# Kernel tuning notes

Measured on AMD Instinct MI355X. Metric: run time of the kernel, lower is better.

Reference implementation:

```python
import jax, jax.numpy as jnp
import numpy as np

SIZE = 128
BATCH = 64
STEEPNESS = 10.0


def _odd_even_indices(n):
    """Odd-even transposition sorting network: n layers of disjoint adjacent pairs.
    All layers are padded to k = n//2 pairs with self-pairs (i,i)=(0,0), which are
    exact no-ops under the soft compare-exchange (matches pass-through wires of the
    original network)."""
    k = n // 2
    ia, ib = [], []
    for layer in range(n):
        start = layer % 2
        pa = list(range(start, n - 1, 2))
        pb = [i + 1 for i in pa]
        while len(pa) < k:  # pad with no-op self-pairs
            pa.append(0)
            pb.append(0)
        ia.append(pa)
        ib.append(pb)
    return jnp.asarray(np.array(ia, np.int32)), jnp.asarray(np.array(ib, np.int32))


def setup_inputs() -> dict:
    key = jax.random.key(0)
    return {"vectors": jax.random.normal(key, (BATCH, SIZE), dtype=jnp.float32)}


def _soft_sort(vectors):
    Bsz, n = vectors.shape
    ia, ib = _odd_even_indices(n)  # [n_layers, k] each
    x0 = vectors
    # X[b, i, j] = soft probability mass of input element i at output slot j,
    # i.e. the invariant  x[b] == vectors[b] @ X[b]  holds after every layer.
    X0 = jnp.tile(jnp.eye(n, dtype=vectors.dtype)[None], (Bsz, 1, 1))
    inv_pi = jnp.float32(1.0 / np.pi)

    def step(carry, idx):
        x, X = carry
        a_idx, b_idx = idx
        a = x[:, a_idx]  # [B, k]
        b = x[:, b_idx]  # [B, k]
        # Cauchy CDF relaxation of the comparison (module default distribution)
        alpha = jnp.arctan(STEEPNESS * (b - a)) * inv_pi + 0.5
        x = x.at[:, a_idx].set(alpha * a + (1.0 - alpha) * b)        # soft min
        x = x.at[:, b_idx].set((1.0 - alpha) * a + alpha * b)        # soft max
        A = X[:, :, a_idx]   # [B, n, k] columns feeding the 'a' wires
        Bc = X[:, :, b_idx]  # [B, n, k] columns feeding the 'b' wires
        w = alpha[:, None, :]
        X = X.at[:, :, a_idx].set(w * A + (1.0 - w) * Bc)
        X = X.at[:, :, b_idx].set((1.0 - w) * A + w * Bc)
        return (x, X), None

    (x, X), _ = jax.lax.scan(step, (x0, X0), (ia, ib))
    return x, X


def reference(vectors):
    # Returns (softly sorted values [B, n], relaxed permutation matrix [B, n, n])
    return _soft_sort(vectors)
```

## Files before the change

### kernel.cpp

```cpp
#include <hip/hip_runtime.h>
#include <math.h>

#define SIZE 128
#define BATCH 64
#define STEEP 10.0f
#define G 8
#define NG 8

template<int CTRL>
__device__ __forceinline__ float dpp_mov(float x) {
    return __int_as_float(__builtin_amdgcn_update_dpp(
        __float_as_int(x), __float_as_int(x), CTRL, 0xf, 0xf, false));
}

__device__ __forceinline__ float alpha_from_delta(float delta) {
    const float C0 =  0.31830265f;
    const float C1 = -0.10587730f;
    const float C2 =  0.06160680f;
    const float C3 = -0.03706173f;
    const float C4 =  0.01676007f;
    const float C5 = -0.00373098f;
    float t  = STEEP * delta;
    float at = fabsf(t);
    bool inv = at > 1.0f;
    float z  = inv ? __builtin_amdgcn_rcpf(at) : at;
    float z2 = z * z, z4 = z2 * z2;
    float p0 = fmaf(C1, z2, C0);
    float p1 = fmaf(C3, z2, C2);
    float p2 = fmaf(C5, z2, C4);
    float q  = fmaf(fmaf(p2, z4, p1), z4, p0) * z;
    float r  = inv ? 0.5f - q : q;
    return 0.5f + copysignf(r, t);
}

__global__ __launch_bounds__(320) void soft_sort_fused(
    const float* __restrict__ vec, float* __restrict__ out)
{
    __shared__ float alds[2][2 * G * 64];

    const int tid    = threadIdx.x;
    const int lane   = tid & 63;
    const int wave   = tid >> 6;
    const int batch  = blockIdx.x >> 2;
    const int rowgrp = blockIdx.x & 3;

    if (wave == 4) {
        const int c0 = 2 * lane;
        const float2 xv = *reinterpret_cast<const float2*>(vec + batch * SIZE + c0);
        float xa = xv.x, xb = xv.y;
        const bool hasR = (lane < 63);
        const bool hasL = (lane > 0);

        for (int grp = 0; grp < NG; ++grp) {
            float* buf = &alds[grp & 1][0];
#pragma unroll
            for (int j = 0; j < G; ++j) {
                const float d  = xb - xa;
                const float ae = alpha_from_delta(d);
                buf[(2 * j) * 64 + lane] = ae;
                const float nxa0 = fmaf(-ae, d, xb);
                const float nxb0 = fmaf( ae, d, xa);
                const float xnext = dpp_mov<0x130>(nxa0);
                float ao = alpha_from_delta(xnext - nxb0);
                ao = hasR ? ao : 1.0f;
                buf[(2 * j + 1) * 64 + lane] = ao;
                float aoL = dpp_mov<0x138>(ao);
                aoL = hasL ? aoL : 1.0f;
                const float xprev = dpp_mov<0x138>(nxb0);
                xb = fmaf(ao,  nxb0 - xnext, xnext);
                xa = fmaf(aoL, nxa0 - xprev, xprev);
            }
            __syncthreads();
        }
        if (rowgrp == 0)
            *reinterpret_cast<float2*>(out + batch * SIZE + c0) = make_float2(xa, xb);
    } else {
        const int chunk = lane & 15;
        const int rsub  = lane >> 4;
        const int row0  = rowgrp * 32 + wave * 8 + rsub * 2;
        const int row1  = row0 + 1;
        const int c8    = chunk * 8;
        const int q4    = chunk * 4;
        const int qm    = (chunk > 0) ? q4 - 1 : 63;

        float va[8], vb[8];
#pragma unroll
        for (int j = 0; j < 8; ++j) {
            va[j] = (row0 == c8 + j) ? 1.0f : 0.0f;
            vb[j] = (row1 == c8 + j) ? 1.0f : 0.0f;
        }

        for (int grp = 0; grp < NG; ++grp) {
            __syncthreads();
            const float* buf = &alds[grp & 1][0];
            float4 ae = *reinterpret_cast<const float4*>(buf + q4);
            float4 ao = *reinterpret_cast<const float4*>(buf + 64 + q4);
            float  aL = buf[64 + qm];
#pragma unroll
            for (int j = 0; j < G; ++j) {
                const int nj = (j < G - 1) ? j + 1 : j;
                const float4 ae_n = *reinterpret_cast<const float4*>(buf + (2 * nj) * 64 + q4);
                const float4 ao_n = *reinterpret_cast<const float4*>(buf + (2 * nj + 1) * 64 + q4);
                const float  aL_n = buf[(2 * nj + 1) * 64 + qm];

                float A, B, d;
                A = va[0]; B = va[1]; d = A - B; va[0] = fmaf(ae.x, d, B); va[1] = fmaf(-ae.x, d, A);
                A = va[2]; B = va[3]; d = A - B; va[2] = fmaf(ae.y, d, B); va[3] = fmaf(-ae.y, d, A);
                A = va[4]; B = va[5]; d = A - B; va[4] = fmaf(ae.z, d, B); va[5] = fmaf(-ae.z, d, A);
                A = va[6]; B = va[7]; d = A - B; va[6] = fmaf(ae.w, d, B); va[7] = fmaf(-ae.w, d, A);
                A = vb[0]; B = vb[1]; d = A - B; vb[0] = fmaf(ae.x, d, B); vb[1] = fmaf(-ae.x, d, A);
                A = vb[2]; B = vb[3]; d = A - B; vb[2] = fmaf(ae.y, d, B); vb[3] = fmaf(-ae.y, d, A);
                A = vb[4]; B = vb[5]; d = A - B; vb[4] = fmaf(ae.z, d, B); vb[5] = fmaf(-ae.z, d, A);
                A = vb[6]; B = vb[7]; d = A - B; vb[6] = fmaf(ae.w, d, B); vb[7] = fmaf(-ae.w, d, A);
                const float nb0a = dpp_mov<0x101>(va[0]);
                const float pb7a = dpp_mov<0x111>(va[7]);
                const float nb0b = dpp_mov<0x101>(vb[0]);
                const float pb7b = dpp_mov<0x111>(vb[7]);
                A = va[1]; B = va[2]; d = A - B; va[1] = fmaf(ao.x, d, B); va[2] = fmaf(-ao.x, d, A);
                A = va[3]; B = va[4]; d = A - B; va[3] = fmaf(ao.y, d, B); va[4] = fmaf(-ao.y, d, A);
                A = va[5]; B = va[6]; d = A - B; va[5] = fmaf(ao.z, d, B); va[6] = fmaf(-ao.z, d, A);
                A = vb[1]; B = vb[2]; d = A - B; vb[1] = fmaf(ao.x, d, B); vb[2] = fmaf(-ao.x, d, A);
                A = vb[3]; B = vb[4]; d = A - B; vb[3] = fmaf(ao.y, d, B); vb[4] = fmaf(-ao.y, d, A);
                A = vb[5]; B = vb[6]; d = A - B; vb[5] = fmaf(ao.z, d, B); vb[6] = fmaf(-ao.z, d, A);
                va[7] = fmaf(ao.w, va[7] - nb0a, nb0a);
                va[0] = fmaf(aL,   va[0] - pb7a, pb7a);
                vb[7] = fmaf(ao.w, vb[7] - nb0b, nb0b);
                vb[0] = fmaf(aL,   vb[0] - pb7b, pb7b);

                ae = ae_n; ao = ao_n; aL = aL_n;
            }
        }

        float* __restrict__ X0 = out + BATCH * SIZE + (batch * SIZE + row0) * SIZE + c8;
        float* __restrict__ X1 = out + BATCH * SIZE + (batch * SIZE + row1) * SIZE + c8;
        *reinterpret_cast<float4*>(X0)     = make_float4(va[0], va[1], va[2], va[3]);
        *reinterpret_cast<float4*>(X0 + 4) = make_float4(va[4], va[5], va[6], va[7]);
        *reinterpret_cast<float4*>(X1)     = make_float4(vb[0], vb[1], vb[2], vb[3]);
        *reinterpret_cast<float4*>(X1 + 4) = make_float4(vb[4], vb[5], vb[6], vb[7]);
    }
}

extern "C" void kernel_launch(void* const* d_in, const int* in_sizes, int n_in,
                              void* d_out, int out_size, void* d_ws, size_t ws_size,
                              hipStream_t stream) {
    const float* vec = (const float*)d_in[0];
    float* out = (float*)d_out;
    (void)in_sizes; (void)n_in; (void)d_ws; (void)ws_size; (void)out_size;

    hipLaunchKernelGGL(soft_sort_fused, dim3(BATCH * 4), dim3(320), 0, stream,
                       vec, out);
}
```

Baseline: 68.75 us.

## Split soft sort into alpha-chain kernel and parallel permutation-evolve kernel via workspace

Replaces the single fused kernel, where one wave computed the alphas while four waves consumed them group by group through double-buffered LDS with barriers, with two kernels. The first kernel runs the sequential alpha chain per batch and writes all alphas to a global workspace. The second kernel loads every alpha for its batch into LDS at once and evolves one row per thread across 512 blocks, with no barriers during the layer loop. This removes the producer/consumer syncs and the serial alpha latency gating the matrix work, at the cost of an extra launch, a global round trip for the alphas, and the full alpha chain now running before any matrix work starts. It falls back to the fused kernel when no workspace is available.

```diff
diff --git a/kernel.cpp b/kernel.cpp
--- a/kernel.cpp
+++ b/kernel.cpp
@@ -6,6 +6,7 @@
 #define STEEP 10.0f
 #define G 8
 #define NG 8
+#define NLP 64
 
 template<int CTRL>
 __device__ __forceinline__ float dpp_mov(float x) {
@@ -31,6 +32,102 @@
     float q  = fmaf(fmaf(p2, z4, p1), z4, p0) * z;
     float r  = inv ? 0.5f - q : q;
     return 0.5f + copysignf(r, t);
+}
+
+__global__ __launch_bounds__(64) void alpha_chain(
+    const float* __restrict__ vec, float* __restrict__ out,
+    float* __restrict__ aws)
+{
+    const int lane  = threadIdx.x;
+    const int batch = blockIdx.x;
+    const int c0    = 2 * lane;
+    const float2 xv = *reinterpret_cast<const float2*>(vec + batch * SIZE + c0);
+    float xa = xv.x, xb = xv.y;
+    const bool hasR = (lane < 63);
+    const bool hasL = (lane > 0);
+    float* __restrict__ w = aws + (size_t)batch * (2 * NLP * 64);
+
+#pragma unroll 8
+    for (int j = 0; j < NLP; ++j) {
+        const float d  = xb - xa;
+        const float ae = alpha_from_delta(d);
+        w[(2 * j) * 64 + lane] = ae;
+        const float nxa0 = fmaf(-ae, d, xb);
+        const float nxb0 = fmaf( ae, d, xa);
+        const float xnext = dpp_mov<0x130>(nxa0);
+        float ao = alpha_from_delta(xnext - nxb0);
+        ao = hasR ? ao : 1.0f;
+        w[(2 * j + 1) * 64 + lane] = ao;
+        float aoL = dpp_mov<0x138>(ao);
+        aoL = hasL ? aoL : 1.0f;
+        const float xprev = dpp_mov<0x138>(nxb0);
+        xb = fmaf(ao,  nxb0 - xnext, xnext);
+        xa = fmaf(aoL, nxa0 - xprev, xprev);
+    }
+    *reinterpret_cast<float2*>(out + batch * SIZE + c0) = make_float2(xa, xb);
+}
+
+__global__ __launch_bounds__(256) void x_evolve(
+    const float* __restrict__ aws, float* __restrict__ out)
+{
+    __shared__ float alds[2 * NLP * 64];
+
+    const int tid    = threadIdx.x;
+    const int batch  = blockIdx.x >> 3;
+    const int rowgrp = blockIdx.x & 7;
+
+    {
+        const float4* s4 = reinterpret_cast<const float4*>(aws + (size_t)batch * 8192);
+        float4* d4 = reinterpret_cast<float4*>(alds);
+#pragma unroll
+        for (int i = 0; i < 8; ++i)
+            d4[i * 256 + tid] = s4[i * 256 + tid];
+    }
+    __syncthreads();
+
+    const int lane  = tid & 63;
+    const int wave  = tid >> 6;
+    const int chunk = lane & 15;
+    const int rsub  = lane >> 4;
+    const int row   = rowgrp * 16 + wave * 4 + rsub;
+    const int c8    = chunk * 8;
+    const int q4    = chunk * 4;
+    const int qm    = (chunk > 0) ? q4 - 1 : 63;
+
+    float v[8];
+#pragma unroll
+    for (int j = 0; j < 8; ++j)
+        v[j] = (row == c8 + j) ? 1.0f : 0.0f;
+
+    float4 ae = *reinterpret_cast<const float4*>(alds + q4);
+    float4 ao = *reinterpret_cast<const float4*>(alds + 64 + q4);
+    float  aL = alds[64 + qm];
+
+    for (int j = 0; j < NLP; ++j) {
+        const int nj = (j < NLP - 1) ? j + 1 : j;
+        const float4 ae_n = *reinterpret_cast<const float4*>(alds + (2 * nj) * 64 + q4);
+        const float4 ao_n = *reinterpret_cast<const float4*>(alds + (2 * nj + 1) * 64 + q4);
+        const float  aL_n = alds[(2 * nj + 1) * 64 + qm];
+
+        float A, B, d;
+        A = v[0]; B = v[1]; d = A - B; v[0] = fmaf(ae.x, d, B); v[1] = fmaf(-ae.x, d, A);
+        A = v[2]; B = v[3]; d = A - B; v[2] = fmaf(ae.y, d, B); v[3] = fmaf(-ae.y, d, A);
+        A = v[4]; B = v[5]; d = A - B; v[4] = fmaf(ae.z, d, B); v[5] = fmaf(-ae.z, d, A);
+        A = v[6]; B = v[7]; d = A - B; v[6] = fmaf(ae.w, d, B); v[7] = fmaf(-ae.w, d, A);
+        const float nb0 = dpp_mov<0x101>(v[0]);
+        const float pb7 = dpp_mov<0x111>(v[7]);
+        A = v[1]; B = v[2]; d = A - B; v[1] = fmaf(ao.x, d, B); v[2] = fmaf(-ao.x, d, A);
+        A = v[3]; B = v[4]; d = A - B; v[3] = fmaf(ao.y, d, B); v[4] = fmaf(-ao.y, d, A);
+        A = v[5]; B = v[6]; d = A - B; v[5] = fmaf(ao.z, d, B); v[6] = fmaf(-ao.z, d, A);
+        v[7] = fmaf(ao.w, v[7] - nb0, nb0);
+        v[0] = fmaf(aL,   v[0] - pb7, pb7);
+
+        ae = ae_n; ao = ao_n; aL = aL_n;
+    }
+
+    float* __restrict__ X = out + BATCH * SIZE + ((size_t)batch * SIZE + row) * SIZE + c8;
+    *reinterpret_cast<float4*>(X)     = make_float4(v[0], v[1], v[2], v[3]);
+    *reinterpret_cast<float4*>(X + 4) = make_float4(v[4], v[5], v[6], v[7]);
 }
 
 __global__ __launch_bounds__(320) void soft_sort_fused(
@@ -145,8 +242,17 @@
                               hipStream_t stream) {
     const float* vec = (const float*)d_in[0];
     float* out = (float*)d_out;
-    (void)in_sizes; (void)n_in; (void)d_ws; (void)ws_size; (void)out_size;
-
-    hipLaunchKernelGGL(soft_sort_fused, dim3(BATCH * 4), dim3(320), 0, stream,
-                       vec, out);
-}
+    (void)in_sizes; (void)n_in; (void)out_size;
+
+    const size_t need = (size_t)BATCH * 2 * NLP * 64 * sizeof(float);
+    if (d_ws != nullptr && ws_size >= need) {
+        float* aws = (float*)d_ws;
+        hipLaunchKernelGGL(alpha_chain, dim3(BATCH), dim3(64), 0, stream,
+                           vec, out, aws);
+        hipLaunchKernelGGL(x_evolve, dim3(BATCH * 8), dim3(256), 0, stream,
+                           aws, out);
+    } else {
+        hipLaunchKernelGGL(soft_sort_fused, dim3(BATCH * 4), dim3(320), 0, stream,
+                           vec, out);
+    }
+}
```

After: 75.97 us. +10.5%, slower.

## Pack row pairs into packed-fp32 vectors and split each batch across more blocks

Applied to the files above, without the earlier changes.

The two rows each lane tracks are now held as 2-wide float vectors, so the compare-exchange updates can map to packed FMA instructions (v_pk_fma_f32) instead of scalar FMAs. Each batch is now split across 8 blocks of 3 waves (2 matrix waves plus 1 alpha-producer wave) instead of 4 blocks of 5 waves, which gives more blocks per batch and shorter per-block work. The alpha-producer wave also raises its scheduling priority so it stays ahead of the consumer waves. The cost is that the serial alpha computation is repeated in twice as many blocks, and the DPP shuffles still run per scalar component.

```diff
diff --git a/kernel.cpp b/kernel.cpp
--- a/kernel.cpp
+++ b/kernel.cpp
@@ -6,6 +6,13 @@
 #define STEEP 10.0f
 #define G 8
 #define NG 8
+
+typedef float v2f __attribute__((ext_vector_type(2)));
+
+__device__ __forceinline__ v2f v2bc(float s) { return (v2f){s, s}; }
+__device__ __forceinline__ v2f v2fma(v2f a, v2f b, v2f c) {
+    return __builtin_elementwise_fma(a, b, c);
+}
 
 template<int CTRL>
 __device__ __forceinline__ float dpp_mov(float x) {
@@ -33,7 +40,7 @@
     return 0.5f + copysignf(r, t);
 }
 
-__global__ __launch_bounds__(320) void soft_sort_fused(
+__global__ __launch_bounds__(192) void soft_sort_fused(
     const float* __restrict__ vec, float* __restrict__ out)
 {
     __shared__ float alds[2][2 * G * 64];
@@ -41,10 +48,11 @@
     const int tid    = threadIdx.x;
     const int lane   = tid & 63;
     const int wave   = tid >> 6;
-    const int batch  = blockIdx.x >> 2;
-    const int rowgrp = blockIdx.x & 3;
+    const int batch  = blockIdx.x >> 3;
+    const int rowgrp = blockIdx.x & 7;
 
-    if (wave == 4) {
+    if (wave == 2) {
+        __builtin_amdgcn_s_setprio(1);
         const int c0 = 2 * lane;
         const float2 xv = *reinterpret_cast<const float2*>(vec + batch * SIZE + c0);
         float xa = xv.x, xb = xv.y;
@@ -77,18 +85,16 @@
     } else {
         const int chunk = lane & 15;
         const int rsub  = lane >> 4;
-        const int row0  = rowgrp * 32 + wave * 8 + rsub * 2;
-        const int row1  = row0 + 1;
+        const int row0  = rowgrp * 16 + wave * 8 + rsub * 2;
         const int c8    = chunk * 8;
         const int q4    = chunk * 4;
         const int qm    = (chunk > 0) ? q4 - 1 : 63;
 
-        float va[8], vb[8];
+        v2f v[8];
 #pragma unroll
-        for (int j = 0; j < 8; ++j) {
-            va[j] = (row0 == c8 + j) ? 1.0f : 0.0f;
-            vb[j] = (row1 == c8 + j) ? 1.0f : 0.0f;
-        }
+        for (int j = 0; j < 8; ++j)
+            v[j] = (v2f){ (row0     == c8 + j) ? 1.0f : 0.0f,
+                          (row0 + 1 == c8 + j) ? 1.0f : 0.0f };
 
         for (int grp = 0; grp < NG; ++grp) {
             __syncthreads();
@@ -103,40 +109,37 @@
                 const float4 ao_n = *reinterpret_cast<const float4*>(buf + (2 * nj + 1) * 64 + q4);
                 const float  aL_n = buf[(2 * nj + 1) * 64 + qm];
 
-                float A, B, d;
-                A = va[0]; B = va[1]; d = A - B; va[0] = fmaf(ae.x, d, B); va[1] = fmaf(-ae.x, d, A);
-                A = va[2]; B = va[3]; d = A - B; va[2] = fmaf(ae.y, d, B); va[3] = fmaf(-ae.y, d, A);
-                A = va[4]; B = va[5]; d = A - B; va[4] = fmaf(ae.z, d, B); va[5] = fmaf(-ae.z, d, A);
-                A = va[6]; B = va[7]; d = A - B; va[6] = fmaf(ae.w, d, B); va[7] = fmaf(-ae.w, d, A);
-                A = vb[0]; B = vb[1]; d = A - B; vb[0] = fmaf(ae.x, d, B); vb[1] = fmaf(-ae.x, d, A);
-                A = vb[2]; B = vb[3]; d = A - B; vb[2] = fmaf(ae.y, d, B); vb[3] = fmaf(-ae.y, d, A);
-                A = vb[4]; B = vb[5]; d = A - B; vb[4] = fmaf(ae.z, d, B); vb[5] = fmaf(-ae.z, d, A);
-                A = vb[6]; B = vb[7]; d = A - B; vb[6] = fmaf(ae.w, d, B); vb[7] = fmaf(-ae.w, d, A);
-                const float nb0a = dpp_mov<0x101>(va[0]);
-                const float pb7a = dpp_mov<0x111>(va[7]);
-                const float nb0b = dpp_mov<0x101>(vb[0]);
-                const float pb7b = dpp_mov<0x111>(vb[7]);
-                A = va[1]; B = va[2]; d = A - B; va[1] = fmaf(ao.x, d, B); va[2] = fmaf(-ao.x, d, A);
-                A = va[3]; B = va[4]; d = A - B; va[3] = fmaf(ao.y, d, B); va[4] = fmaf(-ao.y, d, A);
-                A = va[5]; B = va[6]; d = A - B; va[5] = fmaf(ao.z, d, B); va[6] = fmaf(-ao.z, d, A);
-                A = vb[1]; B = vb[2]; d = A - B; vb[1] = fmaf(ao.x, d, B); vb[2] = fmaf(-ao.x, d, A);
-                A = vb[3]; B = vb[4]; d = A - B; vb[3] = fmaf(ao.y, d, B); vb[4] = fmaf(-ao.y, d, A);
-                A = vb[5]; B = vb[6]; d = A - B; vb[5] = fmaf(ao.z, d, B); vb[6] = fmaf(-ao.z, d, A);
-                va[7] = fmaf(ao.w, va[7] - nb0a, nb0a);
-                va[0] = fmaf(aL,   va[0] - pb7a, pb7a);
-                vb[7] = fmaf(ao.w, vb[7] - nb0b, nb0b);
-                vb[0] = fmaf(aL,   vb[0] - pb7b, pb7b);
+                v2f A, B, d;
+#define CXP(i0, i1, al)                                                        \
+                A = v[i0]; B = v[i1]; d = A - B;                               \
+                v[i0] = v2fma(v2bc(al), d, B);                                 \
+                v[i1] = v2fma(v2bc(-(al)), d, A);
+                CXP(0, 1, ae.x)
+                CXP(2, 3, ae.y)
+                CXP(4, 5, ae.z)
+                CXP(6, 7, ae.w)
+                v2f nb0, pb7;
+                nb0.x = dpp_mov<0x101>(v[0].x);
+                nb0.y = dpp_mov<0x101>(v[0].y);
+                pb7.x = dpp_mov<0x111>(v[7].x);
+                pb7.y = dpp_mov<0x111>(v[7].y);
+                CXP(1, 2, ao.x)
+                CXP(3, 4, ao.y)
+                CXP(5, 6, ao.z)
+#undef CXP
+                v[7] = v2fma(v2bc(ao.w), v[7] - nb0, nb0);
+                v[0] = v2fma(v2bc(aL),   v[0] - pb7, pb7);
 
                 ae = ae_n; ao = ao_n; aL = aL_n;
             }
         }
 
-        float* __restrict__ X0 = out + BATCH * SIZE + (batch * SIZE + row0) * SIZE + c8;
-        float* __restrict__ X1 = out + BATCH * SIZE + (batch * SIZE + row1) * SIZE + c8;
-        *reinterpret_cast<float4*>(X0)     = make_float4(va[0], va[1], va[2], va[3]);
-        *reinterpret_cast<float4*>(X0 + 4) = make_float4(va[4], va[5], va[6], va[7]);
-        *reinterpret_cast<float4*>(X1)     = make_float4(vb[0], vb[1], vb[2], vb[3]);
-        *reinterpret_cast<float4*>(X1 + 4) = make_float4(vb[4], vb[5], vb[6], vb[7]);
+        float* __restrict__ X0 = out + BATCH * SIZE + ((size_t)batch * SIZE + row0) * SIZE + c8;
+        float* __restrict__ X1 = X0 + SIZE;
+        *reinterpret_cast<float4*>(X0)     = make_float4(v[0].x, v[1].x, v[2].x, v[3].x);
+        *reinterpret_cast<float4*>(X0 + 4) = make_float4(v[4].x, v[5].x, v[6].x, v[7].x);
+        *reinterpret_cast<float4*>(X1)     = make_float4(v[0].y, v[1].y, v[2].y, v[3].y);
+        *reinterpret_cast<float4*>(X1 + 4) = make_float4(v[4].y, v[5].y, v[6].y, v[7].y);
     }
 }
 
@@ -147,6 +150,6 @@
     float* out = (float*)d_out;
     (void)in_sizes; (void)n_in; (void)d_ws; (void)ws_size; (void)out_size;
 
-    hipLaunchKernelGGL(soft_sort_fused, dim3(BATCH * 4), dim3(320), 0, stream,
+    hipLaunchKernelGGL(soft_sort_fused, dim3(BATCH * 8), dim3(192), 0, stream,
                        vec, out);
 }
```

Measured after the change: 65.04 us. 1.06x faster.
